# Optimization experiments

Hardware: AMD Instinct MI355X
Metric: run time of the kernel (lower is better)

## Reference

```python
import jax, jax.numpy as jnp
import numpy as np

N_RPN = 4096; N_ROI = 4096
C_RPN = 256; C_ROI = 1024
NOK = 8; NUM_CLASSES = 20
H_RPN = C_RPN // 4; H_ROI = C_ROI // 4
MAX_ITER = 90000; TEMP_CFG = 30.0
EPS = 1e-7


def _attn(x, W1, b1, W2, b2, temp):
    # AttentionLayerWoGP: Linear -> ReLU -> Linear -> softmax(logits / temp)
    h = jax.nn.relu(x @ W1.T + b1)
    return jax.nn.softmax((h @ W2.T + b2) / temp, axis=-1)


def _contrastive(x, temp):
    e = jnp.exp(x / temp)
    # torch: e / (e+eps).sum(dim=1) -> denom shape (N,) broadcasts over LAST axis
    return e / (e + EPS).sum(axis=1)


def _cont_loss(x, gt, temp):
    return -(jnp.log(_contrastive(x, temp)) * _contrastive(gt, temp)).sum(axis=1).mean()


def _forward(rpn_feat, rpn_deltas_in, rpn_scale_in, roi_feat, roi_deltas_in, roi_scale_in,
             W_rpn_feat, b_rpn_feat, W_rpn_del, b_rpn_del, W_rpn_sc, b_rpn_sc,
             W_roi_feat, b_roi_feat, W_roi_del, b_roi_del, W_roi_sc, b_roi_sc,
             rpn_cls_W1, rpn_cls_b1, rpn_cls_W2, rpn_cls_b2,
             rpn_bbox_W1, rpn_bbox_b1, rpn_bbox_W2, rpn_bbox_b2,
             roi_cls_W1, roi_cls_b1, roi_cls_W2, roi_cls_b2,
             rpn_class, roi_class, curr_iter):
    temp = max(1.0, TEMP_CFG * (MAX_ITER - curr_iter) / MAX_ITER)

    rpn_sum = (rpn_feat @ W_rpn_feat.T + b_rpn_feat) \
            + (rpn_deltas_in @ W_rpn_del.T + b_rpn_del) \
            + (rpn_scale_in[:, None] @ W_rpn_sc.T + b_rpn_sc)
    rpn_cls_w, rpn_bbox_w = jnp.split(rpn_sum, 2, axis=-1)
    rpn_cls_alphas = _attn(rpn_cls_w, rpn_cls_W1, rpn_cls_b1, rpn_cls_W2, rpn_cls_b2, temp)
    rpn_bbox_alphas = _attn(rpn_bbox_w, rpn_bbox_W1, rpn_bbox_b1, rpn_bbox_W2, rpn_bbox_b2, temp)

    roi_sum = (roi_feat @ W_roi_feat.T + b_roi_feat) \
            + (roi_deltas_in @ W_roi_del.T + b_roi_del) \
            + (roi_scale_in[:, None] @ W_roi_sc.T + b_roi_sc)
    roi_cls_w, roi_bbox_w = jnp.split(roi_sum, 2, axis=-1)
    roi_cls_alphas = _attn(roi_cls_w, roi_cls_W1, roi_cls_b1, roi_cls_W2, roi_cls_b2, temp)
    # NOTE: original code (bug) reuses roi_cls_alphas module for bbox weights
    roi_bbox_alphas = _attn(roi_bbox_w, roi_cls_W1, roi_cls_b1, roi_cls_W2, roi_cls_b2, temp)

    # contrastive graph losses (NxN matrices)
    roi_cls_gt = (roi_class[None, :] == roi_class[:, None]).astype(jnp.float32)
    rpn_cls_gt = (rpn_class[None, :] == rpn_class[:, None]).astype(jnp.float32)
    roi_bbox_gt = roi_deltas_in @ roi_deltas_in.T
    rpn_bbox_gt = rpn_deltas_in @ rpn_deltas_in.T

    roi_cls_loss = _cont_loss(roi_cls_alphas @ roi_cls_alphas.T, roi_cls_gt, 0.5)
    rpn_cls_loss = _cont_loss(rpn_cls_alphas @ rpn_cls_alphas.T, rpn_cls_gt, 0.5)
    roi_bbox_loss = _cont_loss(roi_bbox_alphas @ roi_bbox_alphas.T, roi_bbox_gt, 0.5)
    rpn_bbox_loss = _cont_loss(rpn_bbox_alphas @ rpn_bbox_alphas.T, rpn_bbox_gt, 0.5)

    # per-class segment mean of roi_cls_alphas (fused replacement of the python loop)
    counts = jax.ops.segment_sum(jnp.ones((N_ROI,), jnp.float32), roi_class, num_segments=NUM_CLASSES)
    sums = jax.ops.segment_sum(roi_cls_alphas, roi_class, num_segments=NUM_CLASSES)
    roi_cls_per_class = sums / jnp.maximum(counts, 1.0)[:, None]  # [NUM_CLASSES, NOK]

    return (rpn_cls_alphas.mean(axis=0),            # [NOK]
            rpn_bbox_alphas.mean(axis=0),           # [NOK]
            roi_cls_per_class,                      # [NUM_CLASSES, NOK]
            roi_bbox_alphas.mean(axis=0)[None, :],  # [1, NOK]
            roi_cls_loss, rpn_cls_loss, roi_bbox_loss, rpn_bbox_loss)


def setup_inputs() -> dict:
    key = jax.random.key(0)
    k = iter(jax.random.split(key, 48))
    def nrm(shape, s=1.0):
        return jax.random.normal(next(k), shape, dtype=jnp.float32) * s
    WS = 0.05
    inp = {}
    inp['rpn_feat'] = nrm((N_RPN, C_RPN))
    inp['rpn_deltas_in'] = nrm((N_RPN, 4))
    inp['rpn_scale_in'] = jax.random.uniform(next(k), (N_RPN,), dtype=jnp.float32)
    inp['roi_feat'] = nrm((N_ROI, C_ROI))
    inp['roi_deltas_in'] = nrm((N_ROI, 4))
    inp['roi_scale_in'] = jax.random.uniform(next(k), (N_ROI,), dtype=jnp.float32)
    inp['rpn_class'] = jax.random.randint(next(k), (N_RPN,), 0, NUM_CLASSES)
    inp['roi_class'] = jax.random.randint(next(k), (N_ROI,), 0, NUM_CLASSES)
    inp['W_rpn_feat'] = nrm((2 * C_RPN, C_RPN), WS); inp['b_rpn_feat'] = jnp.zeros((2 * C_RPN,), jnp.float32)
    inp['W_rpn_del'] = nrm((2 * C_RPN, 4), WS);      inp['b_rpn_del'] = jnp.zeros((2 * C_RPN,), jnp.float32)
    inp['W_rpn_sc'] = nrm((2 * C_RPN, 1), WS);       inp['b_rpn_sc'] = jnp.zeros((2 * C_RPN,), jnp.float32)
    inp['W_roi_feat'] = nrm((2 * C_ROI, C_ROI), WS); inp['b_roi_feat'] = jnp.zeros((2 * C_ROI,), jnp.float32)
    inp['W_roi_del'] = nrm((2 * C_ROI, 4), WS);      inp['b_roi_del'] = jnp.zeros((2 * C_ROI,), jnp.float32)
    inp['W_roi_sc'] = nrm((2 * C_ROI, 1), WS);       inp['b_roi_sc'] = jnp.zeros((2 * C_ROI,), jnp.float32)
    inp['rpn_cls_W1'] = nrm((H_RPN, C_RPN), WS);  inp['rpn_cls_b1'] = jnp.zeros((H_RPN,), jnp.float32)
    inp['rpn_cls_W2'] = nrm((NOK, H_RPN), WS);    inp['rpn_cls_b2'] = jnp.zeros((NOK,), jnp.float32)
    inp['rpn_bbox_W1'] = nrm((H_RPN, C_RPN), WS); inp['rpn_bbox_b1'] = jnp.zeros((H_RPN,), jnp.float32)
    inp['rpn_bbox_W2'] = nrm((NOK, H_RPN), WS);   inp['rpn_bbox_b2'] = jnp.zeros((NOK,), jnp.float32)
    inp['roi_cls_W1'] = nrm((H_ROI, C_ROI), WS);  inp['roi_cls_b1'] = jnp.zeros((H_ROI,), jnp.float32)
    inp['roi_cls_W2'] = nrm((NOK, H_ROI), WS);    inp['roi_cls_b2'] = jnp.zeros((NOK,), jnp.float32)
    inp['curr_iter'] = 10000
    return inp


def reference(rpn_feat, rpn_deltas_in, rpn_scale_in, roi_feat, roi_deltas_in, roi_scale_in,
              rpn_class, roi_class,
              W_rpn_feat, b_rpn_feat, W_rpn_del, b_rpn_del, W_rpn_sc, b_rpn_sc,
              W_roi_feat, b_roi_feat, W_roi_del, b_roi_del, W_roi_sc, b_roi_sc,
              rpn_cls_W1, rpn_cls_b1, rpn_cls_W2, rpn_cls_b2,
              rpn_bbox_W1, rpn_bbox_b1, rpn_bbox_W2, rpn_bbox_b2,
              roi_cls_W1, roi_cls_b1, roi_cls_W2, roi_cls_b2,
              curr_iter):
    return _forward(rpn_feat, rpn_deltas_in, rpn_scale_in, roi_feat, roi_deltas_in, roi_scale_in,
                    W_rpn_feat, b_rpn_feat, W_rpn_del, b_rpn_del, W_rpn_sc, b_rpn_sc,
                    W_roi_feat, b_roi_feat, W_roi_del, b_roi_del, W_roi_sc, b_roi_sc,
                    rpn_cls_W1, rpn_cls_b1, rpn_cls_W2, rpn_cls_b2,
                    rpn_bbox_W1, rpn_bbox_b1, rpn_bbox_W2, rpn_bbox_b2,
                    roi_cls_W1, roi_cls_b1, roi_cls_W2, roi_cls_b2,
                    rpn_class, roi_class, curr_iter)
```

## Files before the change

### kernel.cpp

```cpp
#include <hip/hip_runtime.h>
#include <math.h>

#define NPTS 4096
#define NEPS 4.096e-4f
#define E2   7.3890560989306495f
#define E2M1 6.3890560989306495f

typedef float  f32x4 __attribute__((ext_vector_type(4)));
typedef short  s16x8 __attribute__((ext_vector_type(8)));

static __device__ __forceinline__ unsigned short f2b(float x) {
    unsigned u = __builtin_bit_cast(unsigned, x);
    return (unsigned short)((u + 0x7fffu + ((u >> 16) & 1u)) >> 16);
}
static __device__ __forceinline__ float b2f(unsigned short h) {
    return __builtin_bit_cast(float, (unsigned)h << 16);
}

static __device__ __forceinline__ size_t swz(int r, int c, int R16) {
    return (((size_t)((c >> 5) * R16 + (r >> 4))) << 9)
         + ((size_t)((r & 15) + (((c & 31) >> 3) << 4)) << 3) + (c & 7);
}

__global__ __launch_bounds__(256) void prep_kernel(
    const float* __restrict__ roi_feat, const float* __restrict__ W_roi_feat,
    const float* __restrict__ roi_cls_W1,
    const float* __restrict__ rpn_feat, const float* __restrict__ W_rpn_feat,
    const float* __restrict__ rpn_cls_W1, const float* __restrict__ rpn_bbox_W1,
    const float* __restrict__ rpn_cls_b1, const float* __restrict__ rpn_bbox_b1,
    const float* __restrict__ roi_del, const float* __restrict__ rpn_del,
    unsigned short* __restrict__ roi_feat_sw, unsigned short* __restrict__ W_roi_feat_sw,
    unsigned short* __restrict__ roi_W1_sw,
    unsigned short* __restrict__ rpn_feat_sw, unsigned short* __restrict__ W_rpn_feat_sw,
    unsigned short* __restrict__ rpn_cW1_sw, unsigned short* __restrict__ rpn_bW1_sw,
    unsigned short* __restrict__ Db_roi, unsigned short* __restrict__ Db_rpn,
    float* __restrict__ bias_pad_c, float* __restrict__ bias_pad_b,
    float* __restrict__ out)
{
    const int b = blockIdx.x, t = threadIdx.x;
    if (b < 3776) {
        const float* in; unsigned short* o; int base, cshift, R16;
        if      (b < 2048) { in = roi_feat;   o = roi_feat_sw;   base = b;        cshift = 10; R16 = 256; }
        else if (b < 3072) { in = W_roi_feat; o = W_roi_feat_sw; base = b - 2048; cshift = 10; R16 = 128; }
        else if (b < 3200) { in = roi_cls_W1; o = roi_W1_sw;     base = b - 3072; cshift = 10; R16 = 16;  }
        else if (b < 3712) { in = rpn_feat;   o = rpn_feat_sw;   base = b - 3200; cshift = 8;  R16 = 256; }
        else               { in = W_rpn_feat; o = W_rpn_feat_sw; base = b - 3712; cshift = 8;  R16 = 32;  }
        const int i = base * 2048 + t * 8;
        const int r = i >> cshift, c = i & ((1 << cshift) - 1);
        const float4 v0 = *(const float4*)&in[i];
        const float4 v1 = *(const float4*)&in[i + 4];
        s16x8 pk;
        pk[0] = (short)f2b(v0.x); pk[1] = (short)f2b(v0.y);
        pk[2] = (short)f2b(v0.z); pk[3] = (short)f2b(v0.w);
        pk[4] = (short)f2b(v1.x); pk[5] = (short)f2b(v1.y);
        pk[6] = (short)f2b(v1.z); pk[7] = (short)f2b(v1.w);
        *(s16x8*)(o + swz(r, c, R16)) = pk;
    } else if (b < 3808) {
        const bool cls = b < 3792;
        const float* W = cls ? rpn_cls_W1 : rpn_bbox_W1;
        unsigned short* o = cls ? rpn_cW1_sw : rpn_bW1_sw;
        const int local = b - (cls ? 3776 : 3792);
        const int i = local * 2048 + t * 8;
        const int r = i >> 8, c = i & 255;
        s16x8 pk;
#pragma unroll
        for (int u = 0; u < 8; ++u)
            pk[u] = (r < 64) ? (short)f2b(W[r * 256 + c + u]) : (short)0;
        *(s16x8*)(o + swz(r, c, 8)) = pk;
    } else if (b == 3808) {
        if (t < 128)      bias_pad_c[t] = (t < 64) ? rpn_cls_b1[t] : 0.f;
        else              bias_pad_b[t - 128] = ((t - 128) < 64) ? rpn_bbox_b1[t - 128] : 0.f;
        if (t < 4) out[184 + t] = 0.f;
    } else {
        const int row = (b - 3809) * 256 + t;
        const int mat = row >> 12, r = row & 4095;
        const float* D = mat ? rpn_del : roi_del;
        unsigned short* o = mat ? Db_rpn : Db_roi;
        const float4 dv = *(const float4*)&D[(size_t)r * 4];
        ushort4 d4; d4.x = f2b(dv.x); d4.y = f2b(dv.y); d4.z = f2b(dv.z); d4.w = f2b(dv.w);
        unsigned short* p = o + (size_t)r * 32;
        ushort4 z4 = {0, 0, 0, 0};
        *(ushort4*)p = d4;
        *(ushort4*)(p + 4)  = z4;
        *(ushort4*)(p + 8)  = z4; *(ushort4*)(p + 12) = z4;
        *(ushort4*)(p + 16) = z4; *(ushort4*)(p + 20) = z4;
        *(ushort4*)(p + 24) = z4; *(ushort4*)(p + 28) = z4;
    }
}

struct GemmJob {
    const unsigned short *A, *W;
    unsigned short *C;
    const float *bias;
    const float *del, *Wd, *bd, *sc, *Wsc, *bs;
    int strideA, strideB;
    int M16;
    int ldc;
    int K, nbx, bstart;
    int cw, nchx;
};
struct GemmJobs { GemmJob j[4]; int n; };

#define LDSET(Av, Bv)                                          \
    {                                                          \
        _Pragma("unroll")                                      \
        for (int m = 0; m < 4; ++m) {                          \
            Av[m] = *(const s16x8*)(pa + (m << 9));            \
            Bv[m] = *(const s16x8*)(pb + (m << 9));            \
        }                                                      \
        pa += jb.strideA; pb += jb.strideB;                    \
    }

#define MMSET(Av, Bv)                                          \
    {                                                          \
        _Pragma("unroll")                                      \
        for (int m = 0; m < 4; ++m)                            \
            _Pragma("unroll")                                  \
            for (int n = 0; n < 4; ++n)                        \
                acc[m][n] = __builtin_amdgcn_mfma_f32_16x16x32_bf16( \
                    Av[m], Bv[n], acc[m][n], 0, 0, 0);         \
    }

template<bool EXTRAS, bool CSWZ, bool RELU>
__global__ __launch_bounds__(256) void gemm_reg(GemmJobs jobs)
{
    const int bid = blockIdx.x;
    int ji = 0;
#pragma unroll
    for (int i = 1; i < 4; ++i)
        if (i < jobs.n && bid >= jobs.j[i].bstart) ji = i;
    const GemmJob jb = jobs.j[ji];
    const int local = bid - jb.bstart;
    const int c = local & 7, intra = local >> 3;
    const int ch = (jb.nbx << 2) / jb.cw;
    const int bx = (c % jb.nchx) * jb.cw + intra % jb.cw;
    const int by = (c / jb.nchx) * ch + intra / jb.cw;

    const int t = threadIdx.x, l = t & 63, w = t >> 6;
    const int wr = w >> 1, wc = w & 1;
    const int fr = l & 15, fq = l >> 4;

    const int sA0 = by * 8 + wr * 4;
    const int sB0 = bx * 8 + wc * 4;
    const unsigned short* pa = jb.A + ((size_t)sA0 << 9) + (size_t)(l * 8);
    const unsigned short* pb = jb.W + ((size_t)sB0 << 9) + (size_t)(l * 8);

    f32x4 acc[4][4] = {};
    s16x8 A0[4], B0[4], A1[4], B1[4], A2[4], B2[4], A3[4], B3[4];

    const int niter = jb.K >> 5;
    LDSET(A0, B0);
    LDSET(A1, B1);
    LDSET(A2, B2);

    for (int it = 0; it < niter; it += 4) {
        if (it + 3 < niter) LDSET(A3, B3);
        MMSET(A0, B0);
        if (it + 4 < niter) LDSET(A0, B0);
        MMSET(A1, B1);
        if (it + 5 < niter) LDSET(A1, B1);
        MMSET(A2, B2);
        if (it + 6 < niter) LDSET(A2, B2);
        MMSET(A3, B3);
    }

#pragma unroll
    for (int n = 0; n < 4; ++n) {
        const int cc = (sB0 + n) * 16 + fr;
        float cadd = jb.bias[cc];
        float wd0 = 0.f, wd1 = 0.f, wd2 = 0.f, wd3 = 0.f, wscv = 0.f;
        if (EXTRAS) {
            cadd += jb.bd[cc] + jb.bs[cc];
            const float4 w4 = *(const float4*)&jb.Wd[cc * 4];
            wd0 = w4.x; wd1 = w4.y; wd2 = w4.z; wd3 = w4.w;
            wscv = jb.Wsc[cc];
        }
#pragma unroll
        for (int m = 0; m < 4; ++m) {
            const int si = sA0 + m;
            unsigned short* cp;
            if (CSWZ) {
                const int kj = cc >> 5;
                cp = jb.C + (((size_t)(kj * jb.M16 + si)) << 9)
                   + (((size_t)((cc & 31) >> 3)) << 7) + (cc & 7);
            }
#pragma unroll
            for (int j = 0; j < 4; ++j) {
                const int rr = fq * 4 + j;
                const int row = si * 16 + rr;
                float v = acc[m][n][j] + cadd;
                if (EXTRAS) {
                    const float4 dm = *(const float4*)&jb.del[row * 4];
                    v += dm.x * wd0 + dm.y * wd1 + dm.z * wd2 + dm.w * wd3
                       + jb.sc[row] * wscv;
                }
                if (RELU) v = fmaxf(v, 0.f);
                if (CSWZ) cp[(size_t)rr << 3] = f2b(v);
                else      jb.C[(size_t)row * jb.ldc + cc] = f2b(v);
            }
        }
    }
}

__global__ __launch_bounds__(256) void alphas_all(
    const unsigned short* __restrict__ h_rpn_c, const unsigned short* __restrict__ h_rpn_b,
    const unsigned short* __restrict__ h_roi_c, const unsigned short* __restrict__ h_roi_b,
    const float* __restrict__ W2_rc, const float* __restrict__ W2_rb,
    const float* __restrict__ W2_oc,
    const float* __restrict__ b2_rc, const float* __restrict__ b2_rb,
    const float* __restrict__ b2_oc,
    const int* __restrict__ iter_ptr,
    float* __restrict__ A_rpn_c, float* __restrict__ A_rpn_b,
    float* __restrict__ A_roi_c, float* __restrict__ A_roi_b,
    unsigned short* __restrict__ Ab_all)
{
    const int vrow = blockIdx.x * 4 + (threadIdx.x >> 6);
    const int mat = vrow >> 12, row = vrow & 4095;
    const unsigned short* H; const float *W2, *b2; float* Ao; int ldh, Hd;
    if (mat == 0)      { H = h_rpn_c; W2 = W2_rc; b2 = b2_rc; Ao = A_rpn_c; ldh = 128; Hd = 64; }
    else if (mat == 1) { H = h_rpn_b; W2 = W2_rb; b2 = b2_rb; Ao = A_rpn_b; ldh = 128; Hd = 64; }
    else if (mat == 2) { H = h_roi_c; W2 = W2_oc; b2 = b2_oc; Ao = A_roi_c; ldh = 256; Hd = 256; }
    else               { H = h_roi_b; W2 = W2_oc; b2 = b2_oc; Ao = A_roi_b; ldh = 256; Hd = 256; }

    const int l = threadIdx.x & 63;
    float acc[8] = {};
    for (int m = l * 4; m < Hd; m += 256) {
        const ushort4 h4 = *(const ushort4*)&H[(size_t)row * ldh + m];
        const float h0 = b2f(h4.x), h1 = b2f(h4.y), h2 = b2f(h4.z), h3 = b2f(h4.w);
#pragma unroll
        for (int o = 0; o < 8; ++o) {
            const float4 w4 = *(const float4*)&W2[o * Hd + m];
            acc[o] += h0 * w4.x + h1 * w4.y + h2 * w4.z + h3 * w4.w;
        }
    }
#pragma unroll
    for (int o = 0; o < 8; ++o)
        for (int off = 32; off; off >>= 1)
            acc[o] += __shfl_xor(acc[o], off, 64);

    const int it = *iter_ptr;
    const float temp = fmaxf(1.0f, 30.0f * (float)(90000 - it) / 90000.0f);
    float lg[8], mx = -1e30f;
#pragma unroll
    for (int o = 0; o < 8; ++o) { lg[o] = (acc[o] + b2[o]) / temp; mx = fmaxf(mx, lg[o]); }
    float s = 0.f;
#pragma unroll
    for (int o = 0; o < 8; ++o) { lg[o] = __expf(lg[o] - mx); s += lg[o]; }
    const float inv = 1.0f / s;
    if (l < 8) Ao[(size_t)row * 8 + l] = lg[l] * inv;
    unsigned short* Ab = Ab_all + (size_t)mat * 131072 + (size_t)row * 32;
    if (l == 0) {
        ushort4 o0, o1;
        o0.x = f2b(lg[0]*inv); o0.y = f2b(lg[1]*inv); o0.z = f2b(lg[2]*inv); o0.w = f2b(lg[3]*inv);
        o1.x = f2b(lg[4]*inv); o1.y = f2b(lg[5]*inv); o1.z = f2b(lg[6]*inv); o1.w = f2b(lg[7]*inv);
        *(ushort4*)Ab = o0; *(ushort4*)(Ab + 4) = o1;
    } else if (l < 4) {
        ushort4 z = {0,0,0,0};
        *(ushort4*)(Ab + l * 8)     = z;
        *(ushort4*)(Ab + l * 8 + 4) = z;
    }
}

__global__ __launch_bounds__(256) void finale_kernel(
    const unsigned short* __restrict__ Ab_all,
    const unsigned short* __restrict__ Db_roi, const unsigned short* __restrict__ Db_rpn,
    const float* __restrict__ A_roi_c, const float* __restrict__ A_rpn_c,
    const float* __restrict__ A_roi_b, const float* __restrict__ A_rpn_b,
    const int* __restrict__ roi_class, const int* __restrict__ rpn_class,
    float* __restrict__ part, float* __restrict__ part2, float* __restrict__ out)
{
    const int b = blockIdx.x, t = threadIdx.x;
    const int w = t >> 6, l = t & 63;
    const int fr = l & 15, fq = l >> 4;

    if (b < 512) {
        __shared__ float sh[4][2][16][3];
        const int li = b >> 7;
        const int blk = b & 127;
        const int j0 = blk * 32;
        const bool is_cls = li < 2;
        const int mat = (li == 0) ? 2 : (li == 1) ? 0 : (li == 2) ? 3 : 1;
        const unsigned short* Ab = Ab_all + (size_t)mat * 131072;
        const unsigned short* Db = (li == 2) ? Db_roi : Db_rpn;

        s16x8 bj[2], dj[2];
#pragma unroll
        for (int jt = 0; jt < 2; ++jt) {
            const int j = j0 + jt * 16;
            bj[jt] = *(const s16x8*)&Ab[(size_t)(j + fr) * 32 + fq * 8];
            if (!is_cls) dj[jt] = *(const s16x8*)&Db[(size_t)(j + fr) * 32 + fq * 8];
        }

        float Sx[2] = {}, Sg[2] = {}, U[2] = {};
        const int kbase0 = w * 1024;
        const f32x4 zc = {0.f, 0.f, 0.f, 0.f};

        if (is_cls) {
            for (int ob = 0; ob < 8; ++ob) {
                const int kb0 = kbase0 + ob * 128;
                s16x8 af[8];
#pragma unroll
                for (int u = 0; u < 8; ++u)
                    af[u] = *(const s16x8*)&Ab[(size_t)(kb0 + u * 16 + fr) * 32 + fq * 8];
                f32x4 g[8][2];
#pragma unroll
                for (int u = 0; u < 8; ++u)
#pragma unroll
                    for (int jt = 0; jt < 2; ++jt)
                        g[u][jt] = __builtin_amdgcn_mfma_f32_16x16x32_bf16(af[u], bj[jt], zc, 0, 0, 0);
#pragma unroll
                for (int u = 0; u < 8; ++u)
#pragma unroll
                    for (int jt = 0; jt < 2; ++jt)
#pragma unroll
                        for (int r = 0; r < 4; ++r)
                            Sx[jt] += __expf(2.f * g[u][jt][r]);
            }
        } else {
            for (int ob = 0; ob < 16; ++ob) {
                const int kb0 = kbase0 + ob * 64;
                s16x8 af[4], df[4];
#pragma unroll
                for (int u = 0; u < 4; ++u) {
                    af[u] = *(const s16x8*)&Ab[(size_t)(kb0 + u * 16 + fr) * 32 + fq * 8];
                    df[u] = *(const s16x8*)&Db[(size_t)(kb0 + u * 16 + fr) * 32 + fq * 8];
                }
                f32x4 g[4][2], gd[4][2];
#pragma unroll
                for (int u = 0; u < 4; ++u)
#pragma unroll
                    for (int jt = 0; jt < 2; ++jt) {
                        g[u][jt]  = __builtin_amdgcn_mfma_f32_16x16x32_bf16(af[u], bj[jt], zc, 0, 0, 0);
                        gd[u][jt] = __builtin_amdgcn_mfma_f32_16x16x32_bf16(df[u], dj[jt], zc, 0, 0, 0);
                    }
#pragma unroll
                for (int u = 0; u < 4; ++u)
#pragma unroll
                    for (int jt = 0; jt < 2; ++jt)
#pragma unroll
                        for (int r = 0; r < 4; ++r) {
                            const float gv = g[u][jt][r];
                            const float ed = __expf(2.f * gd[u][jt][r]);
                            Sx[jt] += __expf(2.f * gv);
                            Sg[jt] += ed;
                            U[jt] = fmaf(ed, gv, U[jt]);
                        }
            }
        }

#pragma unroll
        for (int jt = 0; jt < 2; ++jt) {
            float vx = Sx[jt], vg = Sg[jt], vu = U[jt];
            for (int off = 16; off <= 32; off <<= 1) {
                vx += __shfl_xor(vx, off, 64);
                vg += __shfl_xor(vg, off, 64);
                vu += __shfl_xor(vu, off, 64);
            }
            if (fq == 0) {
                sh[w][jt][fr][0] = vx; sh[w][jt][fr][1] = vg; sh[w][jt][fr][2] = vu;
            }
        }
        __syncthreads();
        if (t < 32) {
            const int jt = t >> 4, jl = t & 15;
            float vx = 0.f, vg = 0.f, vu = 0.f;
#pragma unroll
            for (int wv = 0; wv < 4; ++wv) {
                vx += sh[wv][jt][jl][0]; vg += sh[wv][jt][jl][1]; vu += sh[wv][jt][jl][2];
            }
            const int j = j0 + jt * 16 + jl;
            float* p = part + ((size_t)li * 4096 + j) * 3;
            p[0] = vx; p[1] = vg; p[2] = vu;
        }
    } else if (b < 515) {
        __shared__ float S4[4][8];
        const float* A = (b == 512) ? A_rpn_c : (b == 513) ? A_rpn_b : A_roi_b;
        const int off0 = (b == 512) ? 0 : (b == 513) ? 8 : 176;
        float acc[8] = {};
        for (int r = t; r < NPTS; r += 256) {
            const float4 v0 = *(const float4*)&A[(size_t)r * 8];
            const float4 v1 = *(const float4*)&A[(size_t)r * 8 + 4];
            acc[0]+=v0.x; acc[1]+=v0.y; acc[2]+=v0.z; acc[3]+=v0.w;
            acc[4]+=v1.x; acc[5]+=v1.y; acc[6]+=v1.z; acc[7]+=v1.w;
        }
#pragma unroll
        for (int o = 0; o < 8; ++o) {
            float v = acc[o];
            for (int offs = 32; offs; offs >>= 1) v += __shfl_xor(v, offs, 64);
            if (l == 0) S4[w][o] = v;
        }
        __syncthreads();
        if (t < 8) {
            const float s = S4[0][t] + S4[1][t] + S4[2][t] + S4[3][t];
            out[off0 + t] = s * (1.f / 4096.f);
        }
    } else {
        __shared__ float shs[4][20][8];
        __shared__ float shc[4][20];
        const int local = b - 515;
        const int side = local >> 4, blk = local & 15;
        const float* A = side ? A_rpn_c : A_roi_c;
        const int* cls = side ? rpn_class : roi_class;
        const int row = blk * 256 + t;
        const float4 a0 = *(const float4*)&A[(size_t)row * 8];
        const float4 a1 = *(const float4*)&A[(size_t)row * 8 + 4];
        const int myc = cls[row];
#pragma unroll 4
        for (int c = 0; c < 20; ++c) {
            const bool eq = (myc == c);
            float v0 = eq ? a0.x : 0.f, v1 = eq ? a0.y : 0.f;
            float v2 = eq ? a0.z : 0.f, v3 = eq ? a0.w : 0.f;
            float v4 = eq ? a1.x : 0.f, v5 = eq ? a1.y : 0.f;
            float v6 = eq ? a1.z : 0.f, v7 = eq ? a1.w : 0.f;
            float cn = eq ? 1.f : 0.f;
            for (int off = 32; off; off >>= 1) {
                v0 += __shfl_xor(v0, off, 64); v1 += __shfl_xor(v1, off, 64);
                v2 += __shfl_xor(v2, off, 64); v3 += __shfl_xor(v3, off, 64);
                v4 += __shfl_xor(v4, off, 64); v5 += __shfl_xor(v5, off, 64);
                v6 += __shfl_xor(v6, off, 64); v7 += __shfl_xor(v7, off, 64);
                cn += __shfl_xor(cn, off, 64);
            }
            if (l == 0) {
                shs[w][c][0]=v0; shs[w][c][1]=v1; shs[w][c][2]=v2; shs[w][c][3]=v3;
                shs[w][c][4]=v4; shs[w][c][5]=v5; shs[w][c][6]=v6; shs[w][c][7]=v7;
                shc[w][c]=cn;
            }
        }
        __syncthreads();
        float* p2 = part2 + (size_t)(side * 16 + blk) * 192;
        if (t < 160) {
            const int c = t >> 3, o = t & 7;
            p2[t] = shs[0][c][o] + shs[1][c][o] + shs[2][c][o] + shs[3][c][o];
        } else if (t < 180) {
            const int c = t - 160;
            p2[160 + c] = shc[0][c] + shc[1][c] + shc[2][c] + shc[3][c];
        }
    }
}

__global__ __launch_bounds__(256) void loss_finish_kernel(
    const float* __restrict__ part, const float* __restrict__ part2,
    const float* __restrict__ A_roi_c, const float* __restrict__ A_rpn_c,
    const int* __restrict__ roi_class, const int* __restrict__ rpn_class,
    float* __restrict__ out)
{
    const int li = blockIdx.x, t = threadIdx.x;
    __shared__ float V[20][8];
    __shared__ float cnt[20];
    __shared__ float T[8];
    __shared__ float red[4];
    float s = 0.f;
    if (li < 2) {
        const float* A = (li == 0) ? A_roi_c : A_rpn_c;
        const int* cls = (li == 0) ? roi_class : rpn_class;
        const float* p2 = part2 + (size_t)li * 16 * 192;
        if (t < 160) {
            float sv = 0.f;
#pragma unroll
            for (int bb = 0; bb < 16; ++bb) sv += p2[bb * 192 + t];
            V[t >> 3][t & 7] = sv;
        } else if (t >= 192 && t < 212) {
            float cv = 0.f;
#pragma unroll
            for (int bb = 0; bb < 16; ++bb) cv += p2[bb * 192 + 160 + (t - 192)];
            cnt[t - 192] = cv;
        }
        __syncthreads();
        if (li == 0 && t < 160)
            out[16 + t] = V[t >> 3][t & 7] / fmaxf(cnt[t >> 3], 1.f);
        if (t < 8) {
            float tv = 0.f;
            for (int c = 0; c < 20; ++c) tv += V[c][t];
            T[t] = tv;
        }
        __syncthreads();
        if (t < 160) {
            const int c = t >> 3, o = t & 7;
            V[c][o] = T[o] + E2M1 * V[c][o];
        }
        __syncthreads();
#pragma unroll
        for (int u = 0; u < 16; ++u) {
            const int j = t * 16 + u;
            const int c = cls[j];
            const float m = cnt[c];
            const float Cg = (4096.f - m) + m * E2;
            const float4 a0 = *(const float4*)&A[(size_t)j * 8];
            const float4 a1 = *(const float4*)&A[(size_t)j * 8 + 4];
            const float U = a0.x*V[c][0] + a0.y*V[c][1] + a0.z*V[c][2] + a0.w*V[c][3]
                          + a1.x*V[c][4] + a1.y*V[c][5] + a1.z*V[c][6] + a1.w*V[c][7];
            const float Sxj = part[((size_t)li * 4096 + j) * 3];
            s += (2.f * U - __logf(Sxj + NEPS) * Cg) / (Cg + NEPS);
        }
    } else {
#pragma unroll
        for (int u = 0; u < 16; ++u) {
            const int j = t * 16 + u;
            const float* p = part + ((size_t)li * 4096 + j) * 3;
            s += (2.f * p[2] - __logf(p[0] + NEPS) * p[1]) / (p[1] + NEPS);
        }
    }
    for (int off = 32; off; off >>= 1) s += __shfl_xor(s, off, 64);
    if ((t & 63) == 0) red[t >> 6] = s;
    __syncthreads();
    if (t == 0) out[184 + li] = -(red[0] + red[1] + red[2] + red[3]) / 4096.f;
}

extern "C" void kernel_launch(void* const* d_in, const int* in_sizes, int n_in,
                              void* d_out, int out_size, void* d_ws, size_t ws_size,
                              hipStream_t stream)
{
    const float* rpn_feat  = (const float*)d_in[0];
    const float* rpn_del   = (const float*)d_in[1];
    const float* rpn_scale = (const float*)d_in[2];
    const float* roi_feat  = (const float*)d_in[3];
    const float* roi_del   = (const float*)d_in[4];
    const float* roi_scale = (const float*)d_in[5];
    const int*   rpn_class = (const int*)d_in[6];
    const int*   roi_class = (const int*)d_in[7];
    const float* W_rpn_feat = (const float*)d_in[8];  const float* b_rpn_feat = (const float*)d_in[9];
    const float* W_rpn_del  = (const float*)d_in[10]; const float* b_rpn_del  = (const float*)d_in[11];
    const float* W_rpn_sc   = (const float*)d_in[12]; const float* b_rpn_sc   = (const float*)d_in[13];
    const float* W_roi_feat = (const float*)d_in[14]; const float* b_roi_feat = (const float*)d_in[15];
    const float* W_roi_del  = (const float*)d_in[16]; const float* b_roi_del  = (const float*)d_in[17];
    const float* W_roi_sc   = (const float*)d_in[18]; const float* b_roi_sc   = (const float*)d_in[19];
    const float* rpn_cls_W1  = (const float*)d_in[20]; const float* rpn_cls_b1  = (const float*)d_in[21];
    const float* rpn_cls_W2  = (const float*)d_in[22]; const float* rpn_cls_b2  = (const float*)d_in[23];
    const float* rpn_bbox_W1 = (const float*)d_in[24]; const float* rpn_bbox_b1 = (const float*)d_in[25];
    const float* rpn_bbox_W2 = (const float*)d_in[26]; const float* rpn_bbox_b2 = (const float*)d_in[27];
    const float* roi_cls_W1  = (const float*)d_in[28]; const float* roi_cls_b1  = (const float*)d_in[29];
    const float* roi_cls_W2  = (const float*)d_in[30]; const float* roi_cls_b2  = (const float*)d_in[31];
    const int* iter_ptr = (const int*)d_in[32];
    float* out = (float*)d_out;
    char*  wsb = (char*)d_ws;

    unsigned short* roi_feat_sw   = (unsigned short*)(wsb + 0);
    unsigned short* Ab_all        = (unsigned short*)(wsb + 0);
    unsigned short* W_roi_feat_sw = (unsigned short*)(wsb + 8388608);
    float*          part          = (float*)(wsb + 8388608);
    unsigned short* roi_sum_sw    = (unsigned short*)(wsb + 12582912);
    unsigned short* roi_W1_sw     = (unsigned short*)(wsb + 29360128);
    unsigned short* h_roi_c       = (unsigned short*)(wsb + 29884416);
    unsigned short* h_roi_b       = (unsigned short*)(wsb + 31981568);
    unsigned short* rpn_feat_sw   = (unsigned short*)(wsb + 34078720);
    unsigned short* W_rpn_feat_sw = (unsigned short*)(wsb + 36175872);
    unsigned short* rpn_sum_sw    = (unsigned short*)(wsb + 36438016);
    unsigned short* rpn_cW1_sw    = (unsigned short*)(wsb + 40632320);
    unsigned short* rpn_bW1_sw    = (unsigned short*)(wsb + 40697856);
    unsigned short* h_rpn_c       = (unsigned short*)(wsb + 40763392);
    unsigned short* h_rpn_b       = (unsigned short*)(wsb + 41811968);
    float* bias_pad_c = (float*)(wsb + 42860544);
    float* bias_pad_b = (float*)(wsb + 42861056);
    float* A_rpn_c    = (float*)(wsb + 42861568);
    float* A_rpn_b    = (float*)(wsb + 42992640);
    float* A_roi_c    = (float*)(wsb + 43123712);
    float* A_roi_b    = (float*)(wsb + 43254784);
    unsigned short* Db_roi = (unsigned short*)(wsb + 43385856);
    unsigned short* Db_rpn = (unsigned short*)(wsb + 43648000);
    float* part2 = (float*)(wsb + 43910144);

    prep_kernel<<<dim3(3841), 256, 0, stream>>>(
        roi_feat, W_roi_feat, roi_cls_W1, rpn_feat, W_rpn_feat,
        rpn_cls_W1, rpn_bbox_W1, rpn_cls_b1, rpn_bbox_b1,
        roi_del, rpn_del,
        roi_feat_sw, W_roi_feat_sw, roi_W1_sw, rpn_feat_sw, W_rpn_feat_sw,
        rpn_cW1_sw, rpn_bW1_sw, Db_roi, Db_rpn, bias_pad_c, bias_pad_b, out);

    {
        GemmJobs js;
        js.n = 2;
        js.j[0] = { rpn_feat_sw, W_rpn_feat_sw, rpn_sum_sw, b_rpn_feat,
                    rpn_del, W_rpn_del, b_rpn_del, rpn_scale, W_rpn_sc, b_rpn_sc,
                    131072, 16384, 256, 0, 256, 4, 0, 4, 1 };
        js.j[1] = { roi_feat_sw, W_roi_feat_sw, roi_sum_sw, b_roi_feat,
                    roi_del, W_roi_del, b_roi_del, roi_scale, W_roi_sc, b_roi_sc,
                    131072, 65536, 256, 0, 1024, 16, 128, 8, 2 };
        js.j[2] = js.j[0]; js.j[3] = js.j[0];
        gemm_reg<true, true, false><<<dim3(640), 256, 0, stream>>>(js);
    }

    {
        GemmJobs js;
        js.n = 4;
        js.j[0] = { rpn_sum_sw,           rpn_cW1_sw, h_rpn_c, bias_pad_c,
                    nullptr, nullptr, nullptr, nullptr, nullptr, nullptr,
                    131072, 4096, 0, 128, 256, 1, 0, 1, 1 };
        js.j[1] = { rpn_sum_sw + 1048576, rpn_bW1_sw, h_rpn_b, bias_pad_b,
                    nullptr, nullptr, nullptr, nullptr, nullptr, nullptr,
                    131072, 4096, 0, 128, 256, 1, 32, 1, 1 };
        js.j[2] = { roi_sum_sw,           roi_W1_sw, h_roi_c, roi_cls_b1,
                    nullptr, nullptr, nullptr, nullptr, nullptr, nullptr,
                    131072, 8192, 0, 256, 1024, 2, 64, 2, 1 };
        js.j[3] = { roi_sum_sw + 4194304, roi_W1_sw, h_roi_b, roi_cls_b1,
                    nullptr, nullptr, nullptr, nullptr, nullptr, nullptr,
                    131072, 8192, 0, 256, 1024, 2, 128, 2, 1 };
        gemm_reg<false, false, true><<<dim3(192), 256, 0, stream>>>(js);
    }

    alphas_all<<<dim3(4096), 256, 0, stream>>>(
        h_rpn_c, h_rpn_b, h_roi_c, h_roi_b,
        rpn_cls_W2, rpn_bbox_W2, roi_cls_W2,
        rpn_cls_b2, rpn_bbox_b2, roi_cls_b2,
        iter_ptr, A_rpn_c, A_rpn_b, A_roi_c, A_roi_b, Ab_all);

    finale_kernel<<<dim3(547), 256, 0, stream>>>(
        Ab_all, Db_roi, Db_rpn,
        A_roi_c, A_rpn_c, A_roi_b, A_rpn_b,
        roi_class, rpn_class, part, part2, out);

    loss_finish_kernel<<<dim3(4), 256, 0, stream>>>(
        part, part2, A_roi_c, A_rpn_c, roi_class, rpn_class, out);
}
```

Measured before the change: 120.7 us.

## Fold feature projection into first attention layer via precomposed weights

Result: faster. 114.9 us (-4.8%).

```diff
diff --git a/kernel.cpp b/kernel.cpp
--- a/kernel.cpp
+++ b/kernel.cpp
@@ -29,22 +29,28 @@
     const float* __restrict__ rpn_cls_W1, const float* __restrict__ rpn_bbox_W1,
     const float* __restrict__ rpn_cls_b1, const float* __restrict__ rpn_bbox_b1,
     const float* __restrict__ roi_del, const float* __restrict__ rpn_del,
-    unsigned short* __restrict__ roi_feat_sw, unsigned short* __restrict__ W_roi_feat_sw,
+    const float* __restrict__ W_roi_del, const float* __restrict__ W_roi_sc,
+    const float* __restrict__ b_roi_feat, const float* __restrict__ b_roi_del,
+    const float* __restrict__ b_roi_sc,  const float* __restrict__ roi_cls_b1v,
+    const float* __restrict__ W_rpn_del, const float* __restrict__ W_rpn_sc,
+    const float* __restrict__ b_rpn_feat, const float* __restrict__ b_rpn_del,
+    const float* __restrict__ b_rpn_sc,
+    unsigned short* __restrict__ roi_feat_sw,
+    unsigned short* __restrict__ WfT_roi_c, unsigned short* __restrict__ WfT_roi_b,
     unsigned short* __restrict__ roi_W1_sw,
-    unsigned short* __restrict__ rpn_feat_sw, unsigned short* __restrict__ W_rpn_feat_sw,
+    unsigned short* __restrict__ rpn_feat_sw,
+    unsigned short* __restrict__ WfT_rpn_c, unsigned short* __restrict__ WfT_rpn_b,
     unsigned short* __restrict__ rpn_cW1_sw, unsigned short* __restrict__ rpn_bW1_sw,
     unsigned short* __restrict__ Db_roi, unsigned short* __restrict__ Db_rpn,
-    float* __restrict__ bias_pad_c, float* __restrict__ bias_pad_b,
+    float* __restrict__ ext, float* __restrict__ zerobuf,
     float* __restrict__ out)
 {
     const int b = blockIdx.x, t = threadIdx.x;
-    if (b < 3776) {
+    if (b < 2048 || (b >= 3072 && b < 3712)) {
         const float* in; unsigned short* o; int base, cshift, R16;
-        if      (b < 2048) { in = roi_feat;   o = roi_feat_sw;   base = b;        cshift = 10; R16 = 256; }
-        else if (b < 3072) { in = W_roi_feat; o = W_roi_feat_sw; base = b - 2048; cshift = 10; R16 = 128; }
-        else if (b < 3200) { in = roi_cls_W1; o = roi_W1_sw;     base = b - 3072; cshift = 10; R16 = 16;  }
-        else if (b < 3712) { in = rpn_feat;   o = rpn_feat_sw;   base = b - 3200; cshift = 8;  R16 = 256; }
-        else               { in = W_rpn_feat; o = W_rpn_feat_sw; base = b - 3712; cshift = 8;  R16 = 32;  }
+        if      (b < 2048) { in = roi_feat;   o = roi_feat_sw; base = b;        cshift = 10; R16 = 256; }
+        else if (b < 3200) { in = roi_cls_W1; o = roi_W1_sw;   base = b - 3072; cshift = 10; R16 = 16;  }
+        else               { in = rpn_feat;   o = rpn_feat_sw; base = b - 3200; cshift = 8;  R16 = 256; }
         const int i = base * 2048 + t * 8;
         const int r = i >> cshift, c = i & ((1 << cshift) - 1);
         const float4 v0 = *(const float4*)&in[i];
@@ -55,6 +61,30 @@
         pk[4] = (short)f2b(v1.x); pk[5] = (short)f2b(v1.y);
         pk[6] = (short)f2b(v1.z); pk[7] = (short)f2b(v1.w);
         *(s16x8*)(o + swz(r, c, R16)) = pk;
+    } else if (b < 3072) {
+        const int base = b - 2048;
+        const int i = base * 2048 + t * 8;
+        const int o = i >> 10, c0 = i & 1023;
+        unsigned short* dst = (o < 1024) ? WfT_roi_c : WfT_roi_b;
+        const int oo = o & 1023;
+        const float4 v0 = *(const float4*)&W_roi_feat[i];
+        const float4 v1 = *(const float4*)&W_roi_feat[i + 4];
+        const float vv[8] = {v0.x, v0.y, v0.z, v0.w, v1.x, v1.y, v1.z, v1.w};
+#pragma unroll
+        for (int u = 0; u < 8; ++u)
+            dst[swz(c0 + u, oo, 64)] = f2b(vv[u]);
+    } else if (b < 3776) {
+        const int base = b - 3712;
+        const int i = base * 2048 + t * 8;
+        const int o = i >> 8, c0 = i & 255;
+        unsigned short* dst = (o < 256) ? WfT_rpn_c : WfT_rpn_b;
+        const int oo = o & 255;
+        const float4 v0 = *(const float4*)&W_rpn_feat[i];
+        const float4 v1 = *(const float4*)&W_rpn_feat[i + 4];
+        const float vv[8] = {v0.x, v0.y, v0.z, v0.w, v1.x, v1.y, v1.z, v1.w};
+#pragma unroll
+        for (int u = 0; u < 8; ++u)
+            dst[swz(c0 + u, oo, 16)] = f2b(vv[u]);
     } else if (b < 3808) {
         const bool cls = b < 3792;
         const float* W = cls ? rpn_cls_W1 : rpn_bbox_W1;
@@ -67,12 +97,8 @@
         for (int u = 0; u < 8; ++u)
             pk[u] = (r < 64) ? (short)f2b(W[r * 256 + c + u]) : (short)0;
         *(s16x8*)(o + swz(r, c, 8)) = pk;
-    } else if (b == 3808) {
-        if (t < 128)      bias_pad_c[t] = (t < 64) ? rpn_cls_b1[t] : 0.f;
-        else              bias_pad_b[t - 128] = ((t - 128) < 64) ? rpn_bbox_b1[t - 128] : 0.f;
-        if (t < 4) out[184 + t] = 0.f;
-    } else {
-        const int row = (b - 3809) * 256 + t;
+    } else if (b < 3840) {
+        const int row = (b - 3808) * 256 + t;
         const int mat = row >> 12, r = row & 4095;
         const float* D = mat ? rpn_del : roi_del;
         unsigned short* o = mat ? Db_rpn : Db_roi;
@@ -85,6 +111,44 @@
         *(ushort4*)(p + 8)  = z4; *(ushort4*)(p + 12) = z4;
         *(ushort4*)(p + 16) = z4; *(ushort4*)(p + 20) = z4;
         *(ushort4*)(p + 24) = z4; *(ushort4*)(p + 28) = z4;
+    } else if (b < 4096) {
+        const int e = b - 3840;
+        const int job = e >> 6;
+        const int w = t >> 6, l = t & 63;
+        const int hl = (e & 63) * 4 + w;
+        const float *W1, *Wd, *Wsc, *bA, *bB, *bC, *b1;
+        int K, ooff, Hact, Htot;
+        if (job == 0)      { W1 = roi_cls_W1;  K = 1024; ooff = 0;    Wd = W_roi_del; Wsc = W_roi_sc; bA = b_roi_feat; bB = b_roi_del; bC = b_roi_sc; b1 = roi_cls_b1v; Hact = 256; Htot = 256; }
+        else if (job == 1) { W1 = roi_cls_W1;  K = 1024; ooff = 1024; Wd = W_roi_del; Wsc = W_roi_sc; bA = b_roi_feat; bB = b_roi_del; bC = b_roi_sc; b1 = roi_cls_b1v; Hact = 256; Htot = 256; }
+        else if (job == 2) { W1 = rpn_cls_W1;  K = 256;  ooff = 0;    Wd = W_rpn_del; Wsc = W_rpn_sc; bA = b_rpn_feat; bB = b_rpn_del; bC = b_rpn_sc; b1 = rpn_cls_b1;  Hact = 64;  Htot = 128; }
+        else               { W1 = rpn_bbox_W1; K = 256;  ooff = 256;  Wd = W_rpn_del; Wsc = W_rpn_sc; bA = b_rpn_feat; bB = b_rpn_del; bC = b_rpn_sc; b1 = rpn_bbox_b1; Hact = 64;  Htot = 128; }
+        if (hl >= Htot) return;
+        float a0 = 0.f, a1 = 0.f, a2 = 0.f, a3 = 0.f, a4 = 0.f, a5 = 0.f;
+        if (hl < Hact) {
+            for (int o = l; o < K; o += 64) {
+                const float wv = W1[hl * K + o];
+                const float4 wd = *(const float4*)&Wd[(ooff + o) * 4];
+                a0 = fmaf(wv, wd.x, a0); a1 = fmaf(wv, wd.y, a1);
+                a2 = fmaf(wv, wd.z, a2); a3 = fmaf(wv, wd.w, a3);
+                a4 = fmaf(wv, Wsc[ooff + o], a4);
+                a5 = fmaf(wv, bA[ooff + o] + bB[ooff + o] + bC[ooff + o], a5);
+            }
+            for (int off = 32; off; off >>= 1) {
+                a0 += __shfl_xor(a0, off, 64); a1 += __shfl_xor(a1, off, 64);
+                a2 += __shfl_xor(a2, off, 64); a3 += __shfl_xor(a3, off, 64);
+                a4 += __shfl_xor(a4, off, 64); a5 += __shfl_xor(a5, off, 64);
+            }
+        }
+        if (l == 0) {
+            float* ej = ext + job * 1536;
+            ej[hl * 4 + 0] = a0; ej[hl * 4 + 1] = a1;
+            ej[hl * 4 + 2] = a2; ej[hl * 4 + 3] = a3;
+            ej[1024 + hl] = a4;
+            ej[1280 + hl] = (hl < Hact) ? (a5 + b1[hl]) : 0.f;
+        }
+    } else {
+        *(float4*)&zerobuf[t * 4] = float4{0.f, 0.f, 0.f, 0.f};
+        if (t < 4) out[184 + t] = 0.f;
     }
 }
 
@@ -97,7 +161,6 @@
     int M16;
     int ldc;
     int K, nbx, bstart;
-    int cw, nchx;
 };
 struct GemmJobs { GemmJob j[4]; int n; };
 
@@ -131,10 +194,7 @@
         if (i < jobs.n && bid >= jobs.j[i].bstart) ji = i;
     const GemmJob jb = jobs.j[ji];
     const int local = bid - jb.bstart;
-    const int c = local & 7, intra = local >> 3;
-    const int ch = (jb.nbx << 2) / jb.cw;
-    const int bx = (c % jb.nchx) * jb.cw + intra % jb.cw;
-    const int by = (c / jb.nchx) * ch + intra / jb.cw;
+    const int bx = local % jb.nbx, by = local / jb.nbx;
 
     const int t = threadIdx.x, l = t & 63, w = t >> 6;
     const int wr = w >> 1, wc = w & 1;
@@ -534,67 +594,79 @@
     float* out = (float*)d_out;
     char*  wsb = (char*)d_ws;
 
-    unsigned short* roi_feat_sw   = (unsigned short*)(wsb + 0);
-    unsigned short* Ab_all        = (unsigned short*)(wsb + 0);
-    unsigned short* W_roi_feat_sw = (unsigned short*)(wsb + 8388608);
-    float*          part          = (float*)(wsb + 8388608);
-    unsigned short* roi_sum_sw    = (unsigned short*)(wsb + 12582912);
-    unsigned short* roi_W1_sw     = (unsigned short*)(wsb + 29360128);
-    unsigned short* h_roi_c       = (unsigned short*)(wsb + 29884416);
-    unsigned short* h_roi_b       = (unsigned short*)(wsb + 31981568);
-    unsigned short* rpn_feat_sw   = (unsigned short*)(wsb + 34078720);
-    unsigned short* W_rpn_feat_sw = (unsigned short*)(wsb + 36175872);
-    unsigned short* rpn_sum_sw    = (unsigned short*)(wsb + 36438016);
-    unsigned short* rpn_cW1_sw    = (unsigned short*)(wsb + 40632320);
-    unsigned short* rpn_bW1_sw    = (unsigned short*)(wsb + 40697856);
-    unsigned short* h_rpn_c       = (unsigned short*)(wsb + 40763392);
-    unsigned short* h_rpn_b       = (unsigned short*)(wsb + 41811968);
-    float* bias_pad_c = (float*)(wsb + 42860544);
-    float* bias_pad_b = (float*)(wsb + 42861056);
-    float* A_rpn_c    = (float*)(wsb + 42861568);
-    float* A_rpn_b    = (float*)(wsb + 42992640);
-    float* A_roi_c    = (float*)(wsb + 43123712);
-    float* A_roi_b    = (float*)(wsb + 43254784);
+    unsigned short* roi_feat_sw = (unsigned short*)(wsb + 0);
+    unsigned short* Ab_all      = (unsigned short*)(wsb + 0);
+    unsigned short* WfT_roi_c   = (unsigned short*)(wsb + 8388608);
+    unsigned short* WfT_roi_b   = (unsigned short*)(wsb + 10485760);
+    float*          part        = (float*)(wsb + 8388608);
+    unsigned short* comp_roi_c  = (unsigned short*)(wsb + 12582912);
+    unsigned short* comp_roi_b  = (unsigned short*)(wsb + 13107200);
+    unsigned short* comp_rpn_c  = (unsigned short*)(wsb + 13631488);
+    unsigned short* comp_rpn_b  = (unsigned short*)(wsb + 13697024);
+    float*          ext         = (float*)(wsb + 13762560);
+    float*          zerobuf     = (float*)(wsb + 13787136);
+    unsigned short* WfT_rpn_c   = (unsigned short*)(wsb + 13791232);
+    unsigned short* WfT_rpn_b   = (unsigned short*)(wsb + 13922304);
+    unsigned short* roi_W1_sw   = (unsigned short*)(wsb + 29360128);
+    unsigned short* h_roi_c     = (unsigned short*)(wsb + 29884416);
+    unsigned short* h_roi_b     = (unsigned short*)(wsb + 31981568);
+    unsigned short* rpn_feat_sw = (unsigned short*)(wsb + 34078720);
+    unsigned short* rpn_cW1_sw  = (unsigned short*)(wsb + 40632320);
+    unsigned short* rpn_bW1_sw  = (unsigned short*)(wsb + 40697856);
+    unsigned short* h_rpn_c     = (unsigned short*)(wsb + 40763392);
+    unsigned short* h_rpn_b     = (unsigned short*)(wsb + 41811968);
+    float* A_rpn_c = (float*)(wsb + 42861568);
+    float* A_rpn_b = (float*)(wsb + 42992640);
+    float* A_roi_c = (float*)(wsb + 43123712);
+    float* A_roi_b = (float*)(wsb + 43254784);
     unsigned short* Db_roi = (unsigned short*)(wsb + 43385856);
     unsigned short* Db_rpn = (unsigned short*)(wsb + 43648000);
     float* part2 = (float*)(wsb + 43910144);
 
-    prep_kernel<<<dim3(3841), 256, 0, stream>>>(
+    prep_kernel<<<dim3(4097), 256, 0, stream>>>(
         roi_feat, W_roi_feat, roi_cls_W1, rpn_feat, W_rpn_feat,
         rpn_cls_W1, rpn_bbox_W1, rpn_cls_b1, rpn_bbox_b1,
         roi_del, rpn_del,
-        roi_feat_sw, W_roi_feat_sw, roi_W1_sw, rpn_feat_sw, W_rpn_feat_sw,
-        rpn_cW1_sw, rpn_bW1_sw, Db_roi, Db_rpn, bias_pad_c, bias_pad_b, out);
-
-    {
-        GemmJobs js;
-        js.n = 2;
-        js.j[0] = { rpn_feat_sw, W_rpn_feat_sw, rpn_sum_sw, b_rpn_feat,
-                    rpn_del, W_rpn_del, b_rpn_del, rpn_scale, W_rpn_sc, b_rpn_sc,
-                    131072, 16384, 256, 0, 256, 4, 0, 4, 1 };
-        js.j[1] = { roi_feat_sw, W_roi_feat_sw, roi_sum_sw, b_roi_feat,
-                    roi_del, W_roi_del, b_roi_del, roi_scale, W_roi_sc, b_roi_sc,
-                    131072, 65536, 256, 0, 1024, 16, 128, 8, 2 };
-        js.j[2] = js.j[0]; js.j[3] = js.j[0];
-        gemm_reg<true, true, false><<<dim3(640), 256, 0, stream>>>(js);
-    }
+        W_roi_del, W_roi_sc, b_roi_feat, b_roi_del, b_roi_sc, roi_cls_b1,
+        W_rpn_del, W_rpn_sc, b_rpn_feat, b_rpn_del, b_rpn_sc,
+        roi_feat_sw, WfT_roi_c, WfT_roi_b, roi_W1_sw, rpn_feat_sw,
+        WfT_rpn_c, WfT_rpn_b, rpn_cW1_sw, rpn_bW1_sw,
+        Db_roi, Db_rpn, ext, zerobuf, out);
 
     {
         GemmJobs js;
         js.n = 4;
-        js.j[0] = { rpn_sum_sw,           rpn_cW1_sw, h_rpn_c, bias_pad_c,
+        js.j[0] = { roi_W1_sw,  WfT_roi_c, comp_roi_c, zerobuf,
                     nullptr, nullptr, nullptr, nullptr, nullptr, nullptr,
-                    131072, 4096, 0, 128, 256, 1, 0, 1, 1 };
-        js.j[1] = { rpn_sum_sw + 1048576, rpn_bW1_sw, h_rpn_b, bias_pad_b,
+                    8192, 32768, 16, 0, 1024, 8, 0 };
+        js.j[1] = { roi_W1_sw,  WfT_roi_b, comp_roi_b, zerobuf,
                     nullptr, nullptr, nullptr, nullptr, nullptr, nullptr,
-                    131072, 4096, 0, 128, 256, 1, 32, 1, 1 };
-        js.j[2] = { roi_sum_sw,           roi_W1_sw, h_roi_c, roi_cls_b1,
+                    8192, 32768, 16, 0, 1024, 8, 16 };
+        js.j[2] = { rpn_cW1_sw, WfT_rpn_c, comp_rpn_c, zerobuf,
                     nullptr, nullptr, nullptr, nullptr, nullptr, nullptr,
-                    131072, 8192, 0, 256, 1024, 2, 64, 2, 1 };
-        js.j[3] = { roi_sum_sw + 4194304, roi_W1_sw, h_roi_b, roi_cls_b1,
+                    4096, 8192, 8, 0, 256, 2, 32 };
+        js.j[3] = { rpn_bW1_sw, WfT_rpn_b, comp_rpn_b, zerobuf,
                     nullptr, nullptr, nullptr, nullptr, nullptr, nullptr,
-                    131072, 8192, 0, 256, 1024, 2, 128, 2, 1 };
-        gemm_reg<false, false, true><<<dim3(192), 256, 0, stream>>>(js);
+                    4096, 8192, 8, 0, 256, 2, 34 };
+        gemm_reg<false, true, false><<<dim3(36), 256, 0, stream>>>(js);
+    }
+
+    {
+        GemmJobs js;
+        js.n = 4;
+        js.j[0] = { roi_feat_sw, comp_roi_c, h_roi_c, ext + 0 * 1536 + 1280,
+                    roi_del, ext + 0 * 1536, zerobuf, roi_scale, ext + 0 * 1536 + 1024, zerobuf,
+                    131072, 8192, 0, 256, 1024, 2, 0 };
+        js.j[1] = { roi_feat_sw, comp_roi_b, h_roi_b, ext + 1 * 1536 + 1280,
+                    roi_del, ext + 1 * 1536, zerobuf, roi_scale, ext + 1 * 1536 + 1024, zerobuf,
+                    131072, 8192, 0, 256, 1024, 2, 64 };
+        js.j[2] = { rpn_feat_sw, comp_rpn_c, h_rpn_c, ext + 2 * 1536 + 1280,
+                    rpn_del, ext + 2 * 1536, zerobuf, rpn_scale, ext + 2 * 1536 + 1024, zerobuf,
+                    131072, 4096, 0, 128, 256, 1, 128 };
+        js.j[3] = { rpn_feat_sw, comp_rpn_b, h_rpn_b, ext + 3 * 1536 + 1280,
+                    rpn_del, ext + 3 * 1536, zerobuf, rpn_scale, ext + 3 * 1536 + 1024, zerobuf,
+                    131072, 4096, 0, 128, 256, 1, 160 };
+        gemm_reg<true, false, true><<<dim3(192), 256, 0, stream>>>(js);
     }
 
     alphas_all<<<dim3(4096), 256, 0, stream>>>(
```
